# Optimization experiments

Hardware: AMD Instinct MI355X
Metric: run time of the kernel (lower is better)

Reference implementation:

```python
import jax, jax.numpy as jnp
import numpy as np

C = 256
RED = 2
C2 = C // RED


def setup_inputs() -> dict:
    key = jax.random.key(0)
    ks = jax.random.split(key, 6)
    B, H, W = 8, 64, 64
    x = jax.random.normal(ks[0], (B, C, H, W), dtype=jnp.float32)
    # 1x1 convs stored as [out_ch, in_ch] matrices
    W1 = jax.random.normal(ks[1], (C2, C), dtype=jnp.float32) * (1.0 / np.sqrt(C))
    b1 = jax.random.normal(ks[2], (C2,), dtype=jnp.float32) * 0.01
    W2 = jax.random.normal(ks[3], (C, C2), dtype=jnp.float32) * (1.0 / np.sqrt(C2))
    b2 = jax.random.normal(ks[4], (C,), dtype=jnp.float32) * 0.01
    # torch inits scale to zeros; use randn so the residual branch is active
    scale = jax.random.normal(ks[5], (1, C, 1, 1), dtype=jnp.float32)
    return {"x": x, "W1": W1, "b1": b1, "W2": W2, "b2": b2, "scale": scale}


def reference(x, W1, b1, W2, b2, scale):
    B, Cc, H, Wd = x.shape
    # conv1 (1x1): [B,C,H,W] -> [B,C2,H,W]
    y = jnp.einsum('bchw,oc->bohw', x, W1) + b1[None, :, None, None]
    # flatten spatial, move channels last: [B, N, C2]
    y = y.reshape(B, C2, H * Wd).transpose(0, 2, 1)
    # unscaled self-attention over N spatial positions
    att = jax.nn.softmax(jnp.einsum('bmc,bnc->bmn', y, y), axis=-1)  # [B,N,N]
    out = jnp.einsum('bmn,bnc->bmc', att, y)  # [B,N,C2]
    # faithful to torch: raw .view(B,-1,H,W) WITHOUT permuting back
    out = out.reshape(B, C2, H, Wd)
    # conv2 (1x1): [B,C2,H,W] -> [B,C,H,W]
    out = jnp.einsum('bchw,oc->bohw', out, W2) + b2[None, :, None, None]
    return out * scale + x
```

## Files before the change

### kernel.cpp

```cpp
#include <hip/hip_runtime.h>

#define B_  8
#define C_  256
#define C2_ 128
#define N_  4096
#define LOG2E 1.44269504088896f

typedef _Float16 f16;
typedef _Float16 f16x8 __attribute__((ext_vector_type(8)));
typedef float f32x4  __attribute__((ext_vector_type(4)));

static __device__ __forceinline__ unsigned pk2(float a, float b) {
  return __builtin_bit_cast(unsigned, __builtin_amdgcn_cvt_pkrtz(a, b));
}

static __device__ __forceinline__ void plane16_swap(unsigned a, unsigned b,
                                                    unsigned& r0, unsigned& r1) {
#if __has_builtin(__builtin_amdgcn_permlane16_swap)
  auto r = __builtin_amdgcn_permlane16_swap(a, b, false, false);
  r0 = (unsigned)r[0]; r1 = (unsigned)r[1];
#else
  asm volatile("v_permlane16_swap_b32 %0, %1" : "+v"(a), "+v"(b));
  r0 = a; r1 = b;
#endif
}

__global__ __launch_bounds__(256)
void prep_kernel(const float* __restrict__ W1, const float* __restrict__ W2,
                 f16* __restrict__ w1h, f16* __restrict__ w2h)
{
  int i = blockIdx.x * 256 + threadIdx.x;
  w1h[i] = (f16)W1[i];
  w2h[i] = (f16)W2[i];
}

__global__ __launch_bounds__(256, 3)
void conv1_kernel(const float* __restrict__ x,
                  const f16* __restrict__ w1h,
                  const float* __restrict__ b1,
                  f16* __restrict__ Y, f16* __restrict__ Yt)
{
  __shared__ __align__(16) char smem[49152];
  float* Xr = (float*)smem;
  f16*   Ah = (f16*)(smem + 32768);
  f16*   T  = (f16*)smem;

  const int t = threadIdx.x;
  const int w = t >> 6, lane = t & 63, quad = lane >> 4, l16 = lane & 15;
  const int b = blockIdx.x, nt0 = blockIdx.y;

#pragma unroll
  for (int pass = 0; pass < 8; pass++) {
    int c  = (t >> 3) + pass * 32;
    int n4 = t & 7;
    float4 v = *(const float4*)(x + ((long)(b * C_ + c)) * N_ + nt0 * 32 + n4 * 4);
    *(float4*)(&Xr[c * 32 + (n4 ^ (c & 7)) * 4]) = v;
  }
  __syncthreads();
#pragma unroll
  for (int pass = 0; pass < 4; pass++) {
    int n  = t & 31;
    int kb = (t >> 5) + pass * 8;
    f16x8 vh;
#pragma unroll
    for (int jj = 0; jj < 8; jj++) {
      int cc = kb * 8 + jj;
      vh[jj] = (f16)Xr[cc * 32 + ((n >> 2) ^ (cc & 7)) * 4 + (n & 3)];
    }
    *(f16x8*)(&Ah[n * 256 + (kb ^ (n & 7)) * 8]) = vh;
  }
  __syncthreads();

  f16x8 bh[2][8];
#pragma unroll
  for (int nt = 0; nt < 2; nt++) {
    int c2 = w * 32 + nt * 16 + l16;
#pragma unroll
    for (int ks = 0; ks < 8; ks++)
      bh[nt][ks] = *(const f16x8*)(w1h + c2 * C_ + ks * 32 + quad * 8);
  }

  f32x4 acc[2][2];
#pragma unroll
  for (int i = 0; i < 2; i++)
#pragma unroll
    for (int j = 0; j < 2; j++) acc[i][j] = (f32x4){0.f, 0.f, 0.f, 0.f};

#pragma unroll
  for (int ks = 0; ks < 8; ks++)
#pragma unroll
    for (int mt = 0; mt < 2; mt++) {
      f16x8 ah = *(const f16x8*)(&Ah[(mt * 16 + l16) * 256 + (((ks * 4 + quad) ^ (l16 & 7))) * 8]);
#pragma unroll
      for (int nt = 0; nt < 2; nt++)
        acc[mt][nt] = __builtin_amdgcn_mfma_f32_16x16x32_f16(ah, bh[nt][ks], acc[mt][nt], 0, 0, 0);
    }
  __syncthreads();

#pragma unroll
  for (int nt = 0; nt < 2; nt++) {
    int c2 = w * 32 + nt * 16 + l16;
    float bv = b1[c2];
#pragma unroll
    for (int mt = 0; mt < 2; mt++)
#pragma unroll
      for (int rg = 0; rg < 4; rg++) {
        int n = mt * 16 + quad * 4 + rg;
        T[c2 * 40 + n] = (f16)(acc[mt][nt][rg] + bv);
      }
  }
  __syncthreads();
#pragma unroll
  for (int pass = 0; pass < 2; pass++) {
    int r  = (t >> 2) + pass * 64;
    int c8 = (t & 3) * 8;
    f16x8 v = *(const f16x8*)(&T[r * 40 + c8]);
    *(f16x8*)(Yt + ((long)(b * C2_ + r)) * N_ + nt0 * 32 + c8) = v;
  }
#pragma unroll
  for (int pass = 0; pass < 2; pass++) {
    int row = t & 31;
    int cg  = (t >> 5) + pass * 8;
    f16x8 v;
#pragma unroll
    for (int jj = 0; jj < 8; jj++) v[jj] = T[(cg * 8 + jj) * 40 + row];
    *(f16x8*)(Y + ((long)(b * N_ + nt0 * 32 + row)) * C2_ + cg * 8) = v;
  }
}

__global__ __launch_bounds__(256, 2)
void attn_kernel(const f16* __restrict__ Y, const f16* __restrict__ Yt,
                 f16* __restrict__ Op, float* __restrict__ ls)
{
  __shared__ f16 Ks[64 * 128];
  __shared__ f16 Vs[128 * 64];
  __shared__ float nsqf[128];

  const int t = threadIdx.x;
  const int w = t >> 6, lane = t & 63, quad = lane >> 4, l16 = lane & 15;
  const int b = blockIdx.x, qt = blockIdx.y, s = blockIdx.z;
  const int ns = gridDim.z;
  const f16* Yb  = Y  + (long)b * N_ * C2_;
  const f16* Ytb = Yt + (long)b * C2_ * N_;
  const int g0 = (s * 64) / ns;
  const int g1 = ((s + 1) * 64) / ns;

  f16x8 qf[2][4];
#pragma unroll
  for (int mt = 0; mt < 2; mt++)
#pragma unroll
    for (int ks = 0; ks < 4; ks++)
      qf[mt][ks] = *(const f16x8*)(Yb + (long)(qt * 128 + w * 32 + mt * 16 + l16) * C2_ + ks * 32 + quad * 8);

  {
    int r = t >> 1, half = t & 1;
    float ss = 0.f;
#pragma unroll
    for (int j = 0; j < 8; j++) {
      f16x8 v = *(const f16x8*)(Yb + (long)(qt * 128 + r) * C2_ + half * 64 + j * 8);
#pragma unroll
      for (int e = 0; e < 8; e++) { float f = (float)v[e]; ss = fmaf(f, f, ss); }
    }
    ss += __shfl_xor(ss, 1);
    if (!half) nsqf[r] = ss;
  }

  {
    const int kb0 = g0 * 64;
#pragma unroll
    for (int pass = 0; pass < 4; pass++) {
      int r = (t >> 4) + pass * 16;
      f16x8 kv = *(const f16x8*)(Yb + (long)(kb0 + r) * C2_ + (t & 15) * 8);
      *(f16x8*)(&Ks[r * 128 + (((t & 15)) ^ (r & 15)) * 8]) = kv;
    }
#pragma unroll
    for (int pass = 0; pass < 4; pass++) {
      int d = (t >> 3) + pass * 32;
      f16x8 vv = *(const f16x8*)(Ytb + (long)d * N_ + kb0 + (t & 7) * 8);
      *(f16x8*)(&Vs[d * 64 + (((t & 7)) ^ (d & 7)) * 8]) = vv;
    }
  }
  __syncthreads();

  float nm[2];
  nm[0] = nsqf[w * 32 + l16] * LOG2E;
  nm[1] = nsqf[w * 32 + 16 + l16] * LOG2E;

  f16x8 ones8;
#pragma unroll
  for (int j = 0; j < 8; j++) ones8[j] = (f16)1.0f;

  f32x4 Oa[2][8];
#pragma unroll
  for (int i = 0; i < 2; i++)
#pragma unroll
    for (int j = 0; j < 8; j++) Oa[i][j] = (f32x4){0.f, 0.f, 0.f, 0.f};
  f32x4 lac[2] = {(f32x4){0.f,0.f,0.f,0.f}, (f32x4){0.f,0.f,0.f,0.f}};

#pragma unroll 1
  for (int g = g0; g < g1; g++) {
    f16x8 stK[4], stV[4];
    if (g + 1 < g1) {
      int nb = (g + 1) * 64;
#pragma unroll
      for (int pass = 0; pass < 4; pass++)
        stK[pass] = *(const f16x8*)(Yb + (long)(nb + (t >> 4) + pass * 16) * C2_ + (t & 15) * 8);
#pragma unroll
      for (int pass = 0; pass < 4; pass++)
        stV[pass] = *(const f16x8*)(Ytb + (long)((t >> 3) + pass * 32) * N_ + nb + (t & 7) * 8);
    }

    f32x4 S[4][2];
#pragma unroll
    for (int i = 0; i < 4; i++)
#pragma unroll
      for (int j = 0; j < 2; j++) S[i][j] = (f32x4){0.f, 0.f, 0.f, 0.f};
#pragma unroll
    for (int ks = 0; ks < 4; ks++) {
      f16x8 b0 = *(const f16x8*)(&Ks[(0 * 16 + l16) * 128 + (((ks * 4 + quad) ^ l16)) * 8]);
      f16x8 b1 = *(const f16x8*)(&Ks[(1 * 16 + l16) * 128 + (((ks * 4 + quad) ^ l16)) * 8]);
      __builtin_amdgcn_s_setprio(1);
#pragma unroll
      for (int mt = 0; mt < 2; mt++) {
        S[0][mt] = __builtin_amdgcn_mfma_f32_16x16x32_f16(b0, qf[mt][ks], S[0][mt], 0, 0, 0);
        S[1][mt] = __builtin_amdgcn_mfma_f32_16x16x32_f16(b1, qf[mt][ks], S[1][mt], 0, 0, 0);
      }
      __builtin_amdgcn_s_setprio(0);
    }
#pragma unroll
    for (int ks = 0; ks < 4; ks++) {
      f16x8 b2 = *(const f16x8*)(&Ks[(2 * 16 + l16) * 128 + (((ks * 4 + quad) ^ l16)) * 8]);
      f16x8 b3 = *(const f16x8*)(&Ks[(3 * 16 + l16) * 128 + (((ks * 4 + quad) ^ l16)) * 8]);
      __builtin_amdgcn_s_setprio(1);
#pragma unroll
      for (int mt = 0; mt < 2; mt++) {
        S[2][mt] = __builtin_amdgcn_mfma_f32_16x16x32_f16(b2, qf[mt][ks], S[2][mt], 0, 0, 0);
        S[3][mt] = __builtin_amdgcn_mfma_f32_16x16x32_f16(b3, qf[mt][ks], S[3][mt], 0, 0, 0);
      }
      __builtin_amdgcn_s_setprio(0);
    }

    f16x8 pa0[2];
#pragma unroll
    for (int mt = 0; mt < 2; mt++) {
      float n0 = nm[mt];
      unsigned xa0 = pk2(exp2f(fminf(fmaf(S[0][mt][0], LOG2E, -n0), 11.0f)),
                         exp2f(fminf(fmaf(S[0][mt][1], LOG2E, -n0), 11.0f)));
      unsigned xa1 = pk2(exp2f(fminf(fmaf(S[0][mt][2], LOG2E, -n0), 11.0f)),
                         exp2f(fminf(fmaf(S[0][mt][3], LOG2E, -n0), 11.0f)));
      unsigned xb0 = pk2(exp2f(fminf(fmaf(S[1][mt][0], LOG2E, -n0), 11.0f)),
                         exp2f(fminf(fmaf(S[1][mt][1], LOG2E, -n0), 11.0f)));
      unsigned xb1 = pk2(exp2f(fminf(fmaf(S[1][mt][2], LOG2E, -n0), 11.0f)),
                         exp2f(fminf(fmaf(S[1][mt][3], LOG2E, -n0), 11.0f)));
      union { unsigned u[4]; f16x8 v; } P;
      {
        auto c = __builtin_amdgcn_permlane32_swap(xa0, xb0, false, false);
        plane16_swap((unsigned)c[0], (unsigned)c[1], P.u[0], P.u[2]);
      }
      {
        auto c = __builtin_amdgcn_permlane32_swap(xa1, xb1, false, false);
        plane16_swap((unsigned)c[0], (unsigned)c[1], P.u[1], P.u[3]);
      }
      pa0[mt] = P.v;
    }

    {
      f16x8 vb[8];
#pragma unroll
      for (int dt = 0; dt < 8; dt++)
        vb[dt] = *(const f16x8*)(&Vs[(dt * 16 + l16) * 64 + (((0 * 4 + quad) ^ (l16 & 7))) * 8]);
      __builtin_amdgcn_s_setprio(1);
#pragma unroll
      for (int mt = 0; mt < 2; mt++) {
#pragma unroll
        for (int dt = 0; dt < 8; dt++)
          Oa[mt][dt] = __builtin_amdgcn_mfma_f32_16x16x32_f16(pa0[mt], vb[dt], Oa[mt][dt], 0, 0, 0);
        lac[mt] = __builtin_amdgcn_mfma_f32_16x16x32_f16(pa0[mt], ones8, lac[mt], 0, 0, 0);
      }
      __builtin_amdgcn_s_setprio(0);
    }

    f16x8 pa1[2];
#pragma unroll
    for (int mt = 0; mt < 2; mt++) {
      float n0 = nm[mt];
      unsigned xa0 = pk2(exp2f(fminf(fmaf(S[2][mt][0], LOG2E, -n0), 11.0f)),
                         exp2f(fminf(fmaf(S[2][mt][1], LOG2E, -n0), 11.0f)));
      unsigned xa1 = pk2(exp2f(fminf(fmaf(S[2][mt][2], LOG2E, -n0), 11.0f)),
                         exp2f(fminf(fmaf(S[2][mt][3], LOG2E, -n0), 11.0f)));
      unsigned xb0 = pk2(exp2f(fminf(fmaf(S[3][mt][0], LOG2E, -n0), 11.0f)),
                         exp2f(fminf(fmaf(S[3][mt][1], LOG2E, -n0), 11.0f)));
      unsigned xb1 = pk2(exp2f(fminf(fmaf(S[3][mt][2], LOG2E, -n0), 11.0f)),
                         exp2f(fminf(fmaf(S[3][mt][3], LOG2E, -n0), 11.0f)));
      union { unsigned u[4]; f16x8 v; } P;
      {
        auto c = __builtin_amdgcn_permlane32_swap(xa0, xb0, false, false);
        plane16_swap((unsigned)c[0], (unsigned)c[1], P.u[0], P.u[2]);
      }
      {
        auto c = __builtin_amdgcn_permlane32_swap(xa1, xb1, false, false);
        plane16_swap((unsigned)c[0], (unsigned)c[1], P.u[1], P.u[3]);
      }
      pa1[mt] = P.v;
    }

    {
      f16x8 vb[8];
#pragma unroll
      for (int dt = 0; dt < 8; dt++)
        vb[dt] = *(const f16x8*)(&Vs[(dt * 16 + l16) * 64 + (((1 * 4 + quad) ^ (l16 & 7))) * 8]);
      __builtin_amdgcn_s_setprio(1);
#pragma unroll
      for (int mt = 0; mt < 2; mt++) {
#pragma unroll
        for (int dt = 0; dt < 8; dt++)
          Oa[mt][dt] = __builtin_amdgcn_mfma_f32_16x16x32_f16(pa1[mt], vb[dt], Oa[mt][dt], 0, 0, 0);
        lac[mt] = __builtin_amdgcn_mfma_f32_16x16x32_f16(pa1[mt], ones8, lac[mt], 0, 0, 0);
      }
      __builtin_amdgcn_s_setprio(0);
    }

    __syncthreads();
    if (g + 1 < g1) {
#pragma unroll
      for (int pass = 0; pass < 4; pass++) {
        int r = (t >> 4) + pass * 16;
        *(f16x8*)(&Ks[r * 128 + (((t & 15)) ^ (r & 15)) * 8]) = stK[pass];
      }
#pragma unroll
      for (int pass = 0; pass < 4; pass++) {
        int d = (t >> 3) + pass * 32;
        *(f16x8*)(&Vs[d * 64 + (((t & 7)) ^ (d & 7)) * 8]) = stV[pass];
      }
    }
    __syncthreads();
  }

  const long rbase = ((long)s * B_ + b) * N_ + qt * 128;
#pragma unroll
  for (int mt = 0; mt < 2; mt++)
#pragma unroll
    for (int rg = 0; rg < 4; rg++) {
      int r = w * 32 + mt * 16 + quad * 4 + rg;
#pragma unroll
      for (int dt = 0; dt < 8; dt++)
        Op[(rbase + r) * C2_ + dt * 16 + l16] = (f16)Oa[mt][dt][rg];
      if (l16 == 0) ls[rbase + r] = lac[mt][rg];
    }
}

__global__ __launch_bounds__(256, 4)
void conv2_kernel(const f16* __restrict__ Op, const float* __restrict__ ls,
                  const f16* __restrict__ w2h,
                  const float* __restrict__ b2,
                  const float* __restrict__ scale,
                  const float* __restrict__ x,
                  float* __restrict__ out, int ns)
{
  __shared__ f16 Or[128 * 72];
  __shared__ f16 Bsw[64 * 128];
  __shared__ float invL[128];

  const int t = threadIdx.x;
  const int w = t >> 6, lane = t & 63, quad = lane >> 4, l16 = lane & 15;
  const int b = blockIdx.x, pt = blockIdx.y, oh = blockIdx.z;
  const long base0 = (long)b * 524288;

  if (t < 128) {
    int q = t * 32 + (pt >> 1);
    float l = 0.f;
    for (int si = 0; si < ns; si++)
      l += ls[(long)si * 32768 + (long)b * N_ + q];
    invL[t] = 1.0f / fmaxf(l, 1e-20f);
  }
  __syncthreads();

#pragma unroll
  for (int pass = 0; pass < 4; pass++) {
    int j = (t >> 3) + pass * 32;
    int c8 = (t & 7) * 8;
    float fa[8] = {0.f,0.f,0.f,0.f,0.f,0.f,0.f,0.f};
    for (int si = 0; si < ns; si++) {
      f16x8 a = *(const f16x8*)(Op + (long)si * 4194304 + base0 + (long)j * N_ + pt * 64 + c8);
#pragma unroll
      for (int jj = 0; jj < 8; jj++) fa[jj] += (float)a[jj];
    }
    float iv = invL[j];
    f16x8 r;
#pragma unroll
    for (int jj = 0; jj < 8; jj++)
      r[jj] = (f16)(fa[jj] * iv);
    *(f16x8*)(&Or[j * 72 + c8]) = r;
  }
  __syncthreads();
#pragma unroll
  for (int pass = 0; pass < 4; pass++) {
    int p = t & 63;
    int q = (t >> 6) + pass * 4;
    f16x8 vv;
#pragma unroll
    for (int jj = 0; jj < 8; jj++) vv[jj] = Or[(q * 8 + jj) * 72 + p];
    *(f16x8*)(&Bsw[p * 128 + ((q ^ (p & 15))) * 8]) = vv;
  }
  __syncthreads();

  f32x4 acc[2][4];
#pragma unroll
  for (int i = 0; i < 2; i++)
#pragma unroll
    for (int j = 0; j < 4; j++) acc[i][j] = (f32x4){0.f, 0.f, 0.f, 0.f};

#pragma unroll
  for (int ks = 0; ks < 4; ks++) {
    f16x8 bfr[4];
#pragma unroll
    for (int nt = 0; nt < 4; nt++)
      bfr[nt] = *(const f16x8*)(&Bsw[(nt * 16 + l16) * 128 + (((ks * 4 + quad) ^ l16)) * 8]);
#pragma unroll
    for (int mt = 0; mt < 2; mt++) {
      int o = oh * 128 + w * 32 + mt * 16 + l16;
      f16x8 ah = *(const f16x8*)(w2h + o * C2_ + ks * 32 + quad * 8);
#pragma unroll
      for (int nt = 0; nt < 4; nt++)
        acc[mt][nt] = __builtin_amdgcn_mfma_f32_16x16x32_f16(ah, bfr[nt], acc[mt][nt], 0, 0, 0);
    }
  }
#pragma unroll
  for (int mt = 0; mt < 2; mt++)
#pragma unroll
    for (int rg = 0; rg < 4; rg++) {
      int o = oh * 128 + w * 32 + mt * 16 + quad * 4 + rg;
      float so = scale[o], bo = b2[o];
#pragma unroll
      for (int nt = 0; nt < 4; nt++) {
        int p = pt * 64 + nt * 16 + l16;
        long xo = ((long)b * C_ + o) * N_ + p;
        out[xo] = (acc[mt][nt][rg] + bo) * so + x[xo];
      }
    }
}

extern "C" void kernel_launch(void* const* d_in, const int* in_sizes, int n_in,
                              void* d_out, int out_size, void* d_ws, size_t ws_size,
                              hipStream_t stream) {
  const float* x     = (const float*)d_in[0];
  const float* W1    = (const float*)d_in[1];
  const float* b1    = (const float*)d_in[2];
  const float* W2    = (const float*)d_in[3];
  const float* b2    = (const float*)d_in[4];
  const float* scale = (const float*)d_in[5];
  float* outp = (float*)d_out;

  const size_t NE = (size_t)B_ * N_ * C2_;
  const int ns = 2;

  f16* Y   = (f16*)d_ws;
  f16* Yt  = Y + NE;
  f16* Op  = Yt + NE;
  float* ls = (float*)(Op + (size_t)ns * NE);
  f16* w1h = (f16*)(ls + (size_t)ns * 32768);
  f16* w2h = w1h + 32768;

  prep_kernel <<<dim3(128),       dim3(256), 0, stream>>>(W1, W2, w1h, w2h);
  conv1_kernel<<<dim3(8, 128),    dim3(256), 0, stream>>>(x, w1h, b1, Y, Yt);
  attn_kernel <<<dim3(8, 32, ns), dim3(256), 0, stream>>>(Y, Yt, Op, ls);
  conv2_kernel<<<dim3(8, 64, 2),  dim3(256), 0, stream>>>(Op, ls, w2h, b2, scale, x, outp, ns);
}
```

Baseline: 208.7 us.

## Double-buffer K/V tiles in LDS using direct global-to-LDS loads

Replaces the register-staged K/V prefetch with global_load_lds (direct global-to-LDS DMA) into a second LDS buffer, ping-ponging between two buffers each iteration. This removes the staging registers and the ds_write pass, and drops one of the two barriers per iteration. LDS use doubles from 32KB to 64KB per block, which may limit occupancy at 2 blocks/CU. The swizzle moves into the global source addresses. Correctness relies on the barrier and on the compiler's vmcnt waits before the next tile is read, which is a risk.

```diff
diff --git a/kernel.cpp b/kernel.cpp
--- a/kernel.cpp
+++ b/kernel.cpp
@@ -23,6 +23,12 @@
   asm volatile("v_permlane16_swap_b32 %0, %1" : "+v"(a), "+v"(b));
   r0 = a; r1 = b;
 #endif
+}
+
+static __device__ __forceinline__ void gload16(const void* g, void* l) {
+  __builtin_amdgcn_global_load_lds(
+      (const __attribute__((address_space(1))) unsigned int*)g,
+      (__attribute__((address_space(3))) unsigned int*)l, 16, 0, 0);
 }
 
 __global__ __launch_bounds__(256)
@@ -132,8 +138,8 @@
 void attn_kernel(const f16* __restrict__ Y, const f16* __restrict__ Yt,
                  f16* __restrict__ Op, float* __restrict__ ls)
 {
-  __shared__ f16 Ks[64 * 128];
-  __shared__ f16 Vs[128 * 64];
+  __shared__ f16 Ks[2][64 * 128];
+  __shared__ f16 Vs[2][128 * 64];
   __shared__ float nsqf[128];
 
   const int t = threadIdx.x;
@@ -145,6 +151,16 @@
   const int g0 = (s * 64) / ns;
   const int g1 = ((s + 1) * 64) / ns;
 
+  int koff[4], voff[4];
+#pragma unroll
+  for (int i = 0; i < 4; i++) {
+    int p = w + 4 * i;
+    int r = 4 * p + (lane >> 4);
+    koff[i] = r * C2_ + ((l16 ^ (r & 15)) * 8);
+    int d = 8 * p + (lane >> 3);
+    voff[i] = d * N_ + (((lane & 7) ^ (d & 7)) * 8);
+  }
+
   f16x8 qf[2][4];
 #pragma unroll
   for (int mt = 0; mt < 2; mt++)
@@ -167,17 +183,12 @@
 
   {
     const int kb0 = g0 * 64;
-#pragma unroll
-    for (int pass = 0; pass < 4; pass++) {
-      int r = (t >> 4) + pass * 16;
-      f16x8 kv = *(const f16x8*)(Yb + (long)(kb0 + r) * C2_ + (t & 15) * 8);
-      *(f16x8*)(&Ks[r * 128 + (((t & 15)) ^ (r & 15)) * 8]) = kv;
-    }
-#pragma unroll
-    for (int pass = 0; pass < 4; pass++) {
-      int d = (t >> 3) + pass * 32;
-      f16x8 vv = *(const f16x8*)(Ytb + (long)d * N_ + kb0 + (t & 7) * 8);
-      *(f16x8*)(&Vs[d * 64 + (((t & 7)) ^ (d & 7)) * 8]) = vv;
+    const f16* gk = Yb + (long)kb0 * C2_;
+    const f16* gv = Ytb + kb0;
+#pragma unroll
+    for (int i = 0; i < 4; i++) {
+      gload16(gk + koff[i], &Ks[0][(w + 4 * i) * 512]);
+      gload16(gv + voff[i], &Vs[0][(w + 4 * i) * 512]);
     }
   }
   __syncthreads();
@@ -197,17 +208,18 @@
     for (int j = 0; j < 8; j++) Oa[i][j] = (f32x4){0.f, 0.f, 0.f, 0.f};
   f32x4 lac[2] = {(f32x4){0.f,0.f,0.f,0.f}, (f32x4){0.f,0.f,0.f,0.f}};
 
+  int cur = 0;
 #pragma unroll 1
   for (int g = g0; g < g1; g++) {
-    f16x8 stK[4], stV[4];
     if (g + 1 < g1) {
       int nb = (g + 1) * 64;
-#pragma unroll
-      for (int pass = 0; pass < 4; pass++)
-        stK[pass] = *(const f16x8*)(Yb + (long)(nb + (t >> 4) + pass * 16) * C2_ + (t & 15) * 8);
-#pragma unroll
-      for (int pass = 0; pass < 4; pass++)
-        stV[pass] = *(const f16x8*)(Ytb + (long)((t >> 3) + pass * 32) * N_ + nb + (t & 7) * 8);
+      const f16* gk = Yb + (long)nb * C2_;
+      const f16* gv = Ytb + nb;
+#pragma unroll
+      for (int i = 0; i < 4; i++) {
+        gload16(gk + koff[i], &Ks[cur ^ 1][(w + 4 * i) * 512]);
+        gload16(gv + voff[i], &Vs[cur ^ 1][(w + 4 * i) * 512]);
+      }
     }
 
     f32x4 S[4][2];
@@ -217,8 +229,8 @@
       for (int j = 0; j < 2; j++) S[i][j] = (f32x4){0.f, 0.f, 0.f, 0.f};
 #pragma unroll
     for (int ks = 0; ks < 4; ks++) {
-      f16x8 b0 = *(const f16x8*)(&Ks[(0 * 16 + l16) * 128 + (((ks * 4 + quad) ^ l16)) * 8]);
-      f16x8 b1 = *(const f16x8*)(&Ks[(1 * 16 + l16) * 128 + (((ks * 4 + quad) ^ l16)) * 8]);
+      f16x8 b0 = *(const f16x8*)(&Ks[cur][(0 * 16 + l16) * 128 + (((ks * 4 + quad) ^ l16)) * 8]);
+      f16x8 b1 = *(const f16x8*)(&Ks[cur][(1 * 16 + l16) * 128 + (((ks * 4 + quad) ^ l16)) * 8]);
       __builtin_amdgcn_s_setprio(1);
 #pragma unroll
       for (int mt = 0; mt < 2; mt++) {
@@ -229,8 +241,8 @@
     }
 #pragma unroll
     for (int ks = 0; ks < 4; ks++) {
-      f16x8 b2 = *(const f16x8*)(&Ks[(2 * 16 + l16) * 128 + (((ks * 4 + quad) ^ l16)) * 8]);
-      f16x8 b3 = *(const f16x8*)(&Ks[(3 * 16 + l16) * 128 + (((ks * 4 + quad) ^ l16)) * 8]);
+      f16x8 b2 = *(const f16x8*)(&Ks[cur][(2 * 16 + l16) * 128 + (((ks * 4 + quad) ^ l16)) * 8]);
+      f16x8 b3 = *(const f16x8*)(&Ks[cur][(3 * 16 + l16) * 128 + (((ks * 4 + quad) ^ l16)) * 8]);
       __builtin_amdgcn_s_setprio(1);
 #pragma unroll
       for (int mt = 0; mt < 2; mt++) {
@@ -268,7 +280,7 @@
       f16x8 vb[8];
 #pragma unroll
       for (int dt = 0; dt < 8; dt++)
-        vb[dt] = *(const f16x8*)(&Vs[(dt * 16 + l16) * 64 + (((0 * 4 + quad) ^ (l16 & 7))) * 8]);
+        vb[dt] = *(const f16x8*)(&Vs[cur][(dt * 16 + l16) * 64 + (((0 * 4 + quad) ^ (l16 & 7))) * 8]);
       __builtin_amdgcn_s_setprio(1);
 #pragma unroll
       for (int mt = 0; mt < 2; mt++) {
@@ -308,7 +320,7 @@
       f16x8 vb[8];
 #pragma unroll
       for (int dt = 0; dt < 8; dt++)
-        vb[dt] = *(const f16x8*)(&Vs[(dt * 16 + l16) * 64 + (((1 * 4 + quad) ^ (l16 & 7))) * 8]);
+        vb[dt] = *(const f16x8*)(&Vs[cur][(dt * 16 + l16) * 64 + (((1 * 4 + quad) ^ (l16 & 7))) * 8]);
       __builtin_amdgcn_s_setprio(1);
 #pragma unroll
       for (int mt = 0; mt < 2; mt++) {
@@ -321,19 +333,7 @@
     }
 
     __syncthreads();
-    if (g + 1 < g1) {
-#pragma unroll
-      for (int pass = 0; pass < 4; pass++) {
-        int r = (t >> 4) + pass * 16;
-        *(f16x8*)(&Ks[r * 128 + (((t & 15)) ^ (r & 15)) * 8]) = stK[pass];
-      }
-#pragma unroll
-      for (int pass = 0; pass < 4; pass++) {
-        int d = (t >> 3) + pass * 32;
-        *(f16x8*)(&Vs[d * 64 + (((t & 7)) ^ (d & 7)) * 8]) = stV[pass];
-      }
-    }
-    __syncthreads();
+    cur ^= 1;
   }
 
   const long rbase = ((long)s * B_ + b) * N_ + qt * 128;
```

Result: no change. 210.1 us (+0.6%).
